# Kernel tuning notes

Hardware: AMD Instinct MI355X
Metric: run time of the kernel (lower is better)

## Reference

```python
import jax, jax.numpy as jnp
from jax import lax
import numpy as np

IN, H, OUT = 2, 8, 2

def _lstm_layer(x_tbi, w_ih, w_hh, b_ih, b_hh, return_seq):
    # x_tbi: [T, B, in]; w_ih: [4H, in]; w_hh: [4H, H]; biases: [4H]
    T, B, _ = x_tbi.shape
    Hd = w_hh.shape[1]
    # precompute input projection for all timesteps (batched GEMM)
    xs = jnp.einsum('tbi,gi->tbg', x_tbi, w_ih) + (b_ih + b_hh)  # [T, B, 4H]

    def step(carry, xt):
        h, c = carry
        gates = xt + h @ w_hh.T  # [B, 4H]
        i, f, g, o = jnp.split(gates, 4, axis=-1)  # PyTorch gate order i,f,g,o
        i = jax.nn.sigmoid(i)
        f = jax.nn.sigmoid(f)
        g = jnp.tanh(g)
        o = jax.nn.sigmoid(o)
        c = f * c + i * g
        h = o * jnp.tanh(c)
        return (h, c), (h if return_seq else None)

    init = (jnp.zeros((B, Hd), x_tbi.dtype), jnp.zeros((B, Hd), x_tbi.dtype))
    (h_last, _), hs = lax.scan(step, init, xs)
    return hs if return_seq else h_last


def setup_inputs() -> dict:
    key = jax.random.key(0)
    ks = jax.random.split(key, 12)
    s_in = 1.0 / np.sqrt(H)  # PyTorch LSTM init scale U(-1/sqrt(H), 1/sqrt(H))
    def u(k, shape):
        return jax.random.uniform(k, shape, jnp.float32, -s_in, s_in)
    inp = {
        'input': jax.random.normal(ks[0], (32768, 256, IN), jnp.float32),
        'w_ih0': u(ks[1], (4 * H, IN)),
        'w_hh0': u(ks[2], (4 * H, H)),
        'b_ih0': u(ks[3], (4 * H,)),
        'b_hh0': u(ks[4], (4 * H,)),
        'w_ih1': u(ks[5], (4 * H, H)),
        'w_hh1': u(ks[6], (4 * H, H)),
        'b_ih1': u(ks[7], (4 * H,)),
        'b_hh1': u(ks[8], (4 * H,)),
        'w_mlp': u(ks[9], (OUT, H)),
        'b_mlp': u(ks[10], (OUT,)),
    }
    return inp


def reference(input, w_ih0, w_hh0, b_ih0, b_hh0, w_ih1, w_hh1, b_ih1, b_hh1, w_mlp, b_mlp):
    x = jnp.transpose(input, (1, 0, 2))  # [T, B, 2] (batch_first -> time major)
    hs0 = _lstm_layer(x, w_ih0, w_hh0, b_ih0, b_hh0, return_seq=True)   # [T, B, H]
    h1 = _lstm_layer(hs0, w_ih1, w_hh1, b_ih1, b_hh1, return_seq=False)  # [B, H] final step
    return h1 @ w_mlp.T + b_mlp  # [B, 2]
```

## Files before the change

kernel.cpp:

```cpp
#include <hip/hip_runtime.h>


#define TT 256
#define NB 32768

typedef _Float16 half_t;
typedef _Float16 v2h  __attribute__((ext_vector_type(2)));
typedef _Float16 v8h  __attribute__((ext_vector_type(8)));
typedef __fp16   q2h  __attribute__((ext_vector_type(2)));
typedef float    v16f __attribute__((ext_vector_type(16)));
typedef int      v4i  __attribute__((ext_vector_type(4)));

__device__ __forceinline__ v2h pkrtz(float a, float b) {
    q2h r = __builtin_amdgcn_cvt_pkrtz(a, b);
    return __builtin_bit_cast(v2h, r);
}
__device__ __forceinline__ int pk_rtn(float a, float b) {
    v2h v; v.x = (half_t)a; v.y = (half_t)b;
    return __builtin_bit_cast(int, v);
}
__device__ __forceinline__ float rcp_(float x) { return __builtin_amdgcn_rcpf(x); }
__device__ __forceinline__ float ex2_(float x) { return __builtin_amdgcn_exp2f(x); }

__global__ __launch_bounds__(256) void lstm2_mfma32(
    const float* __restrict__ input,
    const float* __restrict__ w_ih0,
    const float* __restrict__ w_hh0,
    const float* __restrict__ b_ih0,
    const float* __restrict__ b_hh0,
    const float* __restrict__ w_ih1,
    const float* __restrict__ w_hh1,
    const float* __restrict__ b_ih1,
    const float* __restrict__ b_hh1,
    const float* __restrict__ w_mlp,
    const float* __restrict__ b_mlp,
    float* __restrict__ out)
{
    const int lane = threadIdx.x & 63;
    const int wave = blockIdx.x * 4 + (threadIdx.x >> 6);
    const int col  = lane & 31;
    const int hf   = lane >> 5;
    const int elem = wave * 32 + col;

    const float L2E = 1.44269504088896f;
    const float NS  = -L2E;
    const float NT2 = -2.0f * L2E;

    const int   row = col;
    const float sA  = (row >= 16 && row < 24) ? NT2 : NS;

    v8h A0, A1;
    if (hf == 0) {
#pragma unroll
        for (int j = 0; j < 8; ++j) {
            A0[j] = (half_t)(sA * w_hh0[row * 8 + j]);
            A1[j] = (half_t)(sA * w_ih1[row * 8 + j]);
        }
    } else {
        A0[0] = (half_t)(sA * w_ih0[row * 2 + 0]);
        A0[1] = (half_t)(sA * w_ih0[row * 2 + 1]);
        A0[2] = A0[0];
        A0[3] = A0[1];
#pragma unroll
        for (int j = 4; j < 8; ++j) A0[j] = (half_t)0.f;
#pragma unroll
        for (int j = 0; j < 8; ++j) A1[j] = (half_t)(sA * w_hh1[row * 8 + j]);
    }

    v16f bias0, bias1;
#pragma unroll
    for (int r = 0; r < 16; ++r) {
        const int   rw = (r & 3) + 8 * (r >> 2) + 4 * hf;
        const float s  = (rw >= 16 && rw < 24) ? NT2 : NS;
        bias0[r] = s * (b_ih0[rw] + b_hh0[rw]);
        bias1[r] = s * (b_ih1[rw] + b_hh1[rw]);
    }

    float c0[4] = {0.f, 0.f, 0.f, 0.f}, c1[4] = {0.f, 0.f, 0.f, 0.f};
    int h0w0 = 0, h0w1 = 0, h0w2 = 0, h0w3 = 0;
    int h1w0 = 0, h1w1 = 0, h1w2 = 0, h1w3 = 0;
    float h1f[4] = {0.f, 0.f, 0.f, 0.f};

    const float4* __restrict__ xp =
        reinterpret_cast<const float4*>(input + (size_t)elem * (TT * 2));

    auto cell = [&](float x0, float x1) {
        v2h xh = pkrtz(x0, x1);
        v2h xl = pkrtz(x0 - (float)xh.x, x1 - (float)xh.y);
        const int xw0 = __builtin_bit_cast(int, xh);
        const int xw1 = __builtin_bit_cast(int, xl);

        v4i b;
        b.x = hf ? xw0 : h0w0;
        b.y = hf ? xw1 : h0w1;
        b.z = hf ? 0   : h0w2;
        b.w = hf ? 0   : h0w3;
        v16f acc = __builtin_amdgcn_mfma_f32_32x32x16_f16(
            A0, __builtin_bit_cast(v8h, b), bias0, 0, 0, 0);

        float nh[4];
#pragma unroll
        for (int j = 0; j < 4; ++j) {
            float ig = rcp_(1.f + ex2_(acc[j]));
            float fg = rcp_(1.f + ex2_(acc[4 + j]));
            float gg = __builtin_fmaf(2.f, rcp_(1.f + ex2_(acc[8 + j])), -1.f);
            float og = rcp_(1.f + ex2_(acc[12 + j]));
            c0[j] = __builtin_fmaf(fg, c0[j], ig * gg);
            float t = __builtin_fmaf(2.f, rcp_(1.f + ex2_(c0[j] * NT2)), -1.f);
            nh[j] = og * t;
        }
        {
            int own0 = pk_rtn(nh[0], nh[1]);
            int own1 = pk_rtn(nh[2], nh[3]);
            int oth0 = __shfl_xor(own0, 32);
            int oth1 = __shfl_xor(own1, 32);
            h0w0 = hf ? oth0 : own0;
            h0w1 = hf ? oth1 : own1;
            h0w2 = hf ? own0 : oth0;
            h0w3 = hf ? own1 : oth1;
        }

        b.x = hf ? h1w0 : h0w0;
        b.y = hf ? h1w1 : h0w1;
        b.z = hf ? h1w2 : h0w2;
        b.w = hf ? h1w3 : h0w3;
        acc = __builtin_amdgcn_mfma_f32_32x32x16_f16(
            A1, __builtin_bit_cast(v8h, b), bias1, 0, 0, 0);

#pragma unroll
        for (int j = 0; j < 4; ++j) {
            float ig = rcp_(1.f + ex2_(acc[j]));
            float fg = rcp_(1.f + ex2_(acc[4 + j]));
            float gg = __builtin_fmaf(2.f, rcp_(1.f + ex2_(acc[8 + j])), -1.f);
            float og = rcp_(1.f + ex2_(acc[12 + j]));
            c1[j] = __builtin_fmaf(fg, c1[j], ig * gg);
            float t = __builtin_fmaf(2.f, rcp_(1.f + ex2_(c1[j] * NT2)), -1.f);
            h1f[j] = og * t;
        }
        {
            int own0 = pk_rtn(h1f[0], h1f[1]);
            int own1 = pk_rtn(h1f[2], h1f[3]);
            int oth0 = __shfl_xor(own0, 32);
            int oth1 = __shfl_xor(own1, 32);
            h1w0 = hf ? oth0 : own0;
            h1w1 = hf ? oth1 : own1;
            h1w2 = hf ? own0 : oth0;
            h1w3 = hf ? own1 : oth1;
        }
    };

    float4 cur = xp[0];
#pragma unroll 1
    for (int it = 0; it < TT / 2; ++it) {
        float4 nxt = xp[(it + 1) & (TT / 2 - 1)];
        cell(cur.x, cur.y);
        cell(cur.z, cur.w);
        cur = nxt;
    }

    const int q = 4 * hf;
    float p0 = 0.f, p1 = 0.f;
#pragma unroll
    for (int j = 0; j < 4; ++j) {
        p0 += w_mlp[q + j] * h1f[j];
        p1 += w_mlp[8 + q + j] * h1f[j];
    }
    p0 += __shfl_xor(p0, 32);
    p1 += __shfl_xor(p1, 32);
    if (hf == 0) {
        out[elem * 2 + 0] = p0 + b_mlp[0];
        out[elem * 2 + 1] = p1 + b_mlp[1];
    }
}

extern "C" void kernel_launch(void* const* d_in, const int* in_sizes, int n_in,
                              void* d_out, int out_size, void* d_ws, size_t ws_size,
                              hipStream_t stream) {
    const float* input = (const float*)d_in[0];
    const float* w_ih0 = (const float*)d_in[1];
    const float* w_hh0 = (const float*)d_in[2];
    const float* b_ih0 = (const float*)d_in[3];
    const float* b_hh0 = (const float*)d_in[4];
    const float* w_ih1 = (const float*)d_in[5];
    const float* w_hh1 = (const float*)d_in[6];
    const float* b_ih1 = (const float*)d_in[7];
    const float* b_hh1 = (const float*)d_in[8];
    const float* w_mlp = (const float*)d_in[9];
    const float* b_mlp = (const float*)d_in[10];
    float* out = (float*)d_out;

    dim3 block(256);
    dim3 grid(NB / 128);
    lstm2_mfma32<<<grid, block, 0, stream>>>(input, w_ih0, w_hh0, b_ih0, b_hh0,
                                             w_ih1, w_hh1, b_ih1, b_hh1,
                                             w_mlp, b_mlp, out);
}
```

Measured before the change: 262.4 us.

## Split LSTM layers across producer/consumer waves with chunked LDS pipeline

Each block now holds two wave pairs. In each pair, one wave runs layer 0 over a 16-step chunk and writes the h0 values to double-buffered shared memory, while the other wave runs layer 1 on the previous chunk. This breaks the serial layer0→layer1 dependency inside one wave, so the two layers' MFMA and transcendental chains can overlap on separate waves. In exchange it needs twice as many waves per element, block-wide barriers every chunk, LDS traffic, and one extra pipeline phase.

```diff
diff --git a/kernel.cpp b/kernel.cpp
--- a/kernel.cpp
+++ b/kernel.cpp
@@ -1,8 +1,10 @@
 #include <hip/hip_runtime.h>
 
 
-#define TT 256
-#define NB 32768
+#define TT  256
+#define NB  32768
+#define CH  16
+#define NCH (TT / CH)
 
 typedef _Float16 half_t;
 typedef _Float16 v2h  __attribute__((ext_vector_type(2)));
@@ -22,7 +24,7 @@
 __device__ __forceinline__ float rcp_(float x) { return __builtin_amdgcn_rcpf(x); }
 __device__ __forceinline__ float ex2_(float x) { return __builtin_amdgcn_exp2f(x); }
 
-__global__ __launch_bounds__(256) void lstm2_mfma32(
+__global__ __launch_bounds__(256) void lstm2_pipe(
     const float* __restrict__ input,
     const float* __restrict__ w_ih0,
     const float* __restrict__ w_hh0,
@@ -37,139 +39,145 @@
     float* __restrict__ out)
 {
     const int lane = threadIdx.x & 63;
-    const int wave = blockIdx.x * 4 + (threadIdx.x >> 6);
+    const int wv   = threadIdx.x >> 6;
+    const int grp  = wv & 1;
+    const int role = wv >> 1;
     const int col  = lane & 31;
     const int hf   = lane >> 5;
-    const int elem = wave * 32 + col;
+    const int elem = blockIdx.x * 64 + grp * 32 + col;
+
+    __shared__ int h0buf[2][2][CH][128];
 
     const float L2E = 1.44269504088896f;
     const float NS  = -L2E;
     const float NT2 = -2.0f * L2E;
-
-    const int   row = col;
-    const float sA  = (row >= 16 && row < 24) ? NT2 : NS;
-
-    v8h A0, A1;
-    if (hf == 0) {
-#pragma unroll
-        for (int j = 0; j < 8; ++j) {
-            A0[j] = (half_t)(sA * w_hh0[row * 8 + j]);
-            A1[j] = (half_t)(sA * w_ih1[row * 8 + j]);
+    const float sA  = (col >= 16 && col < 24) ? NT2 : NS;
+
+    v8h A;
+    if (role == 0) {
+        if (hf == 0) {
+#pragma unroll
+            for (int j = 0; j < 8; ++j) A[j] = (half_t)(sA * w_hh0[col * 8 + j]);
+        } else {
+            A[0] = (half_t)(sA * w_ih0[col * 2 + 0]);
+            A[1] = (half_t)(sA * w_ih0[col * 2 + 1]);
+            A[2] = A[0]; A[3] = A[1];
+#pragma unroll
+            for (int j = 4; j < 8; ++j) A[j] = (half_t)0.f;
         }
     } else {
-        A0[0] = (half_t)(sA * w_ih0[row * 2 + 0]);
-        A0[1] = (half_t)(sA * w_ih0[row * 2 + 1]);
-        A0[2] = A0[0];
-        A0[3] = A0[1];
-#pragma unroll
-        for (int j = 4; j < 8; ++j) A0[j] = (half_t)0.f;
-#pragma unroll
-        for (int j = 0; j < 8; ++j) A1[j] = (half_t)(sA * w_hh1[row * 8 + j]);
-    }
-
-    v16f bias0, bias1;
+        const float* wsrc = hf ? w_hh1 : w_ih1;
+#pragma unroll
+        for (int j = 0; j < 8; ++j) A[j] = (half_t)(sA * wsrc[col * 8 + j]);
+    }
+
+    v16f bias;
 #pragma unroll
     for (int r = 0; r < 16; ++r) {
         const int   rw = (r & 3) + 8 * (r >> 2) + 4 * hf;
         const float s  = (rw >= 16 && rw < 24) ? NT2 : NS;
-        bias0[r] = s * (b_ih0[rw] + b_hh0[rw]);
-        bias1[r] = s * (b_ih1[rw] + b_hh1[rw]);
-    }
-
-    float c0[4] = {0.f, 0.f, 0.f, 0.f}, c1[4] = {0.f, 0.f, 0.f, 0.f};
-    int h0w0 = 0, h0w1 = 0, h0w2 = 0, h0w3 = 0;
-    int h1w0 = 0, h1w1 = 0, h1w2 = 0, h1w3 = 0;
-    float h1f[4] = {0.f, 0.f, 0.f, 0.f};
+        bias[r] = (role == 0) ? s * (b_ih0[rw] + b_hh0[rw])
+                              : s * (b_ih1[rw] + b_hh1[rw]);
+    }
+
+    float c[4] = {0.f, 0.f, 0.f, 0.f};
+    int   hw0 = 0, hw1 = 0, hw2 = 0, hw3 = 0;
+    float hq[4] = {0.f, 0.f, 0.f, 0.f};
 
     const float4* __restrict__ xp =
         reinterpret_cast<const float4*>(input + (size_t)elem * (TT * 2));
 
-    auto cell = [&](float x0, float x1) {
-        v2h xh = pkrtz(x0, x1);
-        v2h xl = pkrtz(x0 - (float)xh.x, x1 - (float)xh.y);
-        const int xw0 = __builtin_bit_cast(int, xh);
-        const int xw1 = __builtin_bit_cast(int, xl);
-
-        v4i b;
-        b.x = hf ? xw0 : h0w0;
-        b.y = hf ? xw1 : h0w1;
-        b.z = hf ? 0   : h0w2;
-        b.w = hf ? 0   : h0w3;
-        v16f acc = __builtin_amdgcn_mfma_f32_32x32x16_f16(
-            A0, __builtin_bit_cast(v8h, b), bias0, 0, 0, 0);
-
-        float nh[4];
+    auto gates = [&](const v16f& acc, float* hout) {
 #pragma unroll
         for (int j = 0; j < 4; ++j) {
             float ig = rcp_(1.f + ex2_(acc[j]));
             float fg = rcp_(1.f + ex2_(acc[4 + j]));
             float gg = __builtin_fmaf(2.f, rcp_(1.f + ex2_(acc[8 + j])), -1.f);
             float og = rcp_(1.f + ex2_(acc[12 + j]));
-            c0[j] = __builtin_fmaf(fg, c0[j], ig * gg);
-            float t = __builtin_fmaf(2.f, rcp_(1.f + ex2_(c0[j] * NT2)), -1.f);
-            nh[j] = og * t;
-        }
-        {
-            int own0 = pk_rtn(nh[0], nh[1]);
-            int own1 = pk_rtn(nh[2], nh[3]);
-            int oth0 = __shfl_xor(own0, 32);
-            int oth1 = __shfl_xor(own1, 32);
-            h0w0 = hf ? oth0 : own0;
-            h0w1 = hf ? oth1 : own1;
-            h0w2 = hf ? own0 : oth0;
-            h0w3 = hf ? own1 : oth1;
-        }
-
-        b.x = hf ? h1w0 : h0w0;
-        b.y = hf ? h1w1 : h0w1;
-        b.z = hf ? h1w2 : h0w2;
-        b.w = hf ? h1w3 : h0w3;
-        acc = __builtin_amdgcn_mfma_f32_32x32x16_f16(
-            A1, __builtin_bit_cast(v8h, b), bias1, 0, 0, 0);
-
+            c[j] = __builtin_fmaf(fg, c[j], ig * gg);
+            float t = __builtin_fmaf(2.f, rcp_(1.f + ex2_(c[j] * NT2)), -1.f);
+            hout[j] = og * t;
+        }
+    };
+
+    for (int ph = 0; ph <= NCH; ++ph) {
+        if (role == 0) {
+            if (ph < NCH) {
+                int* lb = &h0buf[grp][ph & 1][0][0];
+#pragma unroll 2
+                for (int s2 = 0; s2 < CH / 2; ++s2) {
+                    float4 xv = xp[ph * (CH / 2) + s2];
+#pragma unroll
+                    for (int half = 0; half < 2; ++half) {
+                        float x0 = half ? xv.z : xv.x;
+                        float x1 = half ? xv.w : xv.y;
+                        v2h xh = pkrtz(x0, x1);
+                        v2h xl = pkrtz(x0 - (float)xh.x, x1 - (float)xh.y);
+                        int xw0 = __builtin_bit_cast(int, xh);
+                        int xw1 = __builtin_bit_cast(int, xl);
+                        v4i b;
+                        b.x = hf ? xw0 : hw0;
+                        b.y = hf ? xw1 : hw1;
+                        b.z = hf ? 0   : hw2;
+                        b.w = hf ? 0   : hw3;
+                        v16f acc = __builtin_amdgcn_mfma_f32_32x32x16_f16(
+                            A, __builtin_bit_cast(v8h, b), bias, 0, 0, 0);
+                        float nh[4];
+                        gates(acc, nh);
+                        int own0 = pk_rtn(nh[0], nh[1]);
+                        int own1 = pk_rtn(nh[2], nh[3]);
+                        int2 st; st.x = own0; st.y = own1;
+                        *reinterpret_cast<int2*>(
+                            &lb[(2 * s2 + half) * 128 + col * 4 + hf * 2]) = st;
+                        int oth0 = __shfl_xor(own0, 32);
+                        int oth1 = __shfl_xor(own1, 32);
+                        hw0 = hf ? oth0 : own0;
+                        hw1 = hf ? oth1 : own1;
+                        hw2 = hf ? own0 : oth0;
+                        hw3 = hf ? own1 : oth1;
+                    }
+                }
+            }
+        } else if (ph > 0) {
+            const int* lb = &h0buf[grp][(ph - 1) & 1][0][0];
+#pragma unroll 2
+            for (int s = 0; s < CH; ++s) {
+                v4i hh = *reinterpret_cast<const v4i*>(&lb[s * 128 + col * 4]);
+                v4i b;
+                b.x = hf ? hw0 : hh.x;
+                b.y = hf ? hw1 : hh.y;
+                b.z = hf ? hw2 : hh.z;
+                b.w = hf ? hw3 : hh.w;
+                v16f acc = __builtin_amdgcn_mfma_f32_32x32x16_f16(
+                    A, __builtin_bit_cast(v8h, b), bias, 0, 0, 0);
+                gates(acc, hq);
+                int own0 = pk_rtn(hq[0], hq[1]);
+                int own1 = pk_rtn(hq[2], hq[3]);
+                int oth0 = __shfl_xor(own0, 32);
+                int oth1 = __shfl_xor(own1, 32);
+                hw0 = hf ? oth0 : own0;
+                hw1 = hf ? oth1 : own1;
+                hw2 = hf ? own0 : oth0;
+                hw3 = hf ? own1 : oth1;
+            }
+        }
+        __syncthreads();
+    }
+
+    if (role == 1) {
+        const int q = 4 * hf;
+        float p0 = 0.f, p1 = 0.f;
 #pragma unroll
         for (int j = 0; j < 4; ++j) {
-            float ig = rcp_(1.f + ex2_(acc[j]));
-            float fg = rcp_(1.f + ex2_(acc[4 + j]));
-            float gg = __builtin_fmaf(2.f, rcp_(1.f + ex2_(acc[8 + j])), -1.f);
-            float og = rcp_(1.f + ex2_(acc[12 + j]));
-            c1[j] = __builtin_fmaf(fg, c1[j], ig * gg);
-            float t = __builtin_fmaf(2.f, rcp_(1.f + ex2_(c1[j] * NT2)), -1.f);
-            h1f[j] = og * t;
-        }
-        {
-            int own0 = pk_rtn(h1f[0], h1f[1]);
-            int own1 = pk_rtn(h1f[2], h1f[3]);
-            int oth0 = __shfl_xor(own0, 32);
-            int oth1 = __shfl_xor(own1, 32);
-            h1w0 = hf ? oth0 : own0;
-            h1w1 = hf ? oth1 : own1;
-            h1w2 = hf ? own0 : oth0;
-            h1w3 = hf ? own1 : oth1;
-        }
-    };
-
-    float4 cur = xp[0];
-#pragma unroll 1
-    for (int it = 0; it < TT / 2; ++it) {
-        float4 nxt = xp[(it + 1) & (TT / 2 - 1)];
-        cell(cur.x, cur.y);
-        cell(cur.z, cur.w);
-        cur = nxt;
-    }
-
-    const int q = 4 * hf;
-    float p0 = 0.f, p1 = 0.f;
-#pragma unroll
-    for (int j = 0; j < 4; ++j) {
-        p0 += w_mlp[q + j] * h1f[j];
-        p1 += w_mlp[8 + q + j] * h1f[j];
-    }
-    p0 += __shfl_xor(p0, 32);
-    p1 += __shfl_xor(p1, 32);
-    if (hf == 0) {
-        out[elem * 2 + 0] = p0 + b_mlp[0];
-        out[elem * 2 + 1] = p1 + b_mlp[1];
+            p0 += w_mlp[q + j] * hq[j];
+            p1 += w_mlp[8 + q + j] * hq[j];
+        }
+        p0 += __shfl_xor(p0, 32);
+        p1 += __shfl_xor(p1, 32);
+        if (hf == 0) {
+            out[elem * 2 + 0] = p0 + b_mlp[0];
+            out[elem * 2 + 1] = p1 + b_mlp[1];
+        }
     }
 }
 
@@ -190,8 +198,8 @@
     float* out = (float*)d_out;
 
     dim3 block(256);
-    dim3 grid(NB / 128);
-    lstm2_mfma32<<<grid, block, 0, stream>>>(input, w_ih0, w_hh0, b_ih0, b_hh0,
-                                             w_ih1, w_hh1, b_ih1, b_hh1,
-                                             w_mlp, b_mlp, out);
-}
+    dim3 grid(NB / 64);
+    lstm2_pipe<<<grid, block, 0, stream>>>(input, w_ih0, w_hh0, b_ih0, b_hh0,
+                                           w_ih1, w_hh1, b_ih1, b_hh1,
+                                           w_mlp, b_mlp, out);
+}
```

After: 256.6 us. 1.02x faster.

## Skew layer pipeline and remap MFMA K-split to drop lane shuffles

Applied to the files above, without the earlier changes.

The two LSTM layers are now software-pipelined with a one-step skew. Layer 0 at step t and layer 1 at step t-1 are issued as independent MFMAs, then both gate activations run, so the dependency chains can overlap. The A-operand layout is reorganized so each half-wave supplies K-slices that match the h values it already holds. This removes the per-step cross-half shuffles and selects that the old layout needed. A prologue and epilogue handle the skew, and the rearranged K layout must stay numerically equivalent.

```diff
diff --git a/kernel.cpp b/kernel.cpp
--- a/kernel.cpp
+++ b/kernel.cpp
@@ -22,7 +22,7 @@
 __device__ __forceinline__ float rcp_(float x) { return __builtin_amdgcn_rcpf(x); }
 __device__ __forceinline__ float ex2_(float x) { return __builtin_amdgcn_exp2f(x); }
 
-__global__ __launch_bounds__(256) void lstm2_mfma32(
+__global__ __launch_bounds__(256) void lstm2_dual(
     const float* __restrict__ input,
     const float* __restrict__ w_ih0,
     const float* __restrict__ w_hh0,
@@ -45,26 +45,22 @@
     const float L2E = 1.44269504088896f;
     const float NS  = -L2E;
     const float NT2 = -2.0f * L2E;
-
     const int   row = col;
     const float sA  = (row >= 16 && row < 24) ? NT2 : NS;
 
     v8h A0, A1;
+#pragma unroll
+    for (int j = 0; j < 4; ++j) {
+        A0[j]     = (half_t)(sA * w_hh0[row * 8 + 4 * hf + j]);
+        A1[j]     = (half_t)(sA * w_ih1[row * 8 + 4 * hf + j]);
+        A1[4 + j] = (half_t)(sA * w_hh1[row * 8 + 4 * hf + j]);
+    }
     if (hf == 0) {
-#pragma unroll
-        for (int j = 0; j < 8; ++j) {
-            A0[j] = (half_t)(sA * w_hh0[row * 8 + j]);
-            A1[j] = (half_t)(sA * w_ih1[row * 8 + j]);
-        }
+        A0[4] = (half_t)(sA * w_ih0[row * 2 + 0]);
+        A0[5] = (half_t)(sA * w_ih0[row * 2 + 1]);
+        A0[6] = A0[4]; A0[7] = A0[5];
     } else {
-        A0[0] = (half_t)(sA * w_ih0[row * 2 + 0]);
-        A0[1] = (half_t)(sA * w_ih0[row * 2 + 1]);
-        A0[2] = A0[0];
-        A0[3] = A0[1];
-#pragma unroll
-        for (int j = 4; j < 8; ++j) A0[j] = (half_t)0.f;
-#pragma unroll
-        for (int j = 0; j < 8; ++j) A1[j] = (half_t)(sA * w_hh1[row * 8 + j]);
+        A0[4] = A0[5] = A0[6] = A0[7] = (half_t)0.f;
     }
 
     v16f bias0, bias1;
@@ -77,85 +73,78 @@
     }
 
     float c0[4] = {0.f, 0.f, 0.f, 0.f}, c1[4] = {0.f, 0.f, 0.f, 0.f};
-    int h0w0 = 0, h0w1 = 0, h0w2 = 0, h0w3 = 0;
-    int h1w0 = 0, h1w1 = 0, h1w2 = 0, h1w3 = 0;
+    int   h0w0 = 0, h0w1 = 0;
+    int   h1w0 = 0, h1w1 = 0;
     float h1f[4] = {0.f, 0.f, 0.f, 0.f};
 
     const float4* __restrict__ xp =
         reinterpret_cast<const float4*>(input + (size_t)elem * (TT * 2));
 
-    auto cell = [&](float x0, float x1) {
-        v2h xh = pkrtz(x0, x1);
-        v2h xl = pkrtz(x0 - (float)xh.x, x1 - (float)xh.y);
-        const int xw0 = __builtin_bit_cast(int, xh);
-        const int xw1 = __builtin_bit_cast(int, xl);
-
-        v4i b;
-        b.x = hf ? xw0 : h0w0;
-        b.y = hf ? xw1 : h0w1;
-        b.z = hf ? 0   : h0w2;
-        b.w = hf ? 0   : h0w3;
-        v16f acc = __builtin_amdgcn_mfma_f32_32x32x16_f16(
-            A0, __builtin_bit_cast(v8h, b), bias0, 0, 0, 0);
-
-        float nh[4];
+    auto gates = [&](const v16f& acc, float* c, float* hout) {
 #pragma unroll
         for (int j = 0; j < 4; ++j) {
             float ig = rcp_(1.f + ex2_(acc[j]));
             float fg = rcp_(1.f + ex2_(acc[4 + j]));
             float gg = __builtin_fmaf(2.f, rcp_(1.f + ex2_(acc[8 + j])), -1.f);
             float og = rcp_(1.f + ex2_(acc[12 + j]));
-            c0[j] = __builtin_fmaf(fg, c0[j], ig * gg);
-            float t = __builtin_fmaf(2.f, rcp_(1.f + ex2_(c0[j] * NT2)), -1.f);
-            nh[j] = og * t;
-        }
-        {
-            int own0 = pk_rtn(nh[0], nh[1]);
-            int own1 = pk_rtn(nh[2], nh[3]);
-            int oth0 = __shfl_xor(own0, 32);
-            int oth1 = __shfl_xor(own1, 32);
-            h0w0 = hf ? oth0 : own0;
-            h0w1 = hf ? oth1 : own1;
-            h0w2 = hf ? own0 : oth0;
-            h0w3 = hf ? own1 : oth1;
-        }
-
-        b.x = hf ? h1w0 : h0w0;
-        b.y = hf ? h1w1 : h0w1;
-        b.z = hf ? h1w2 : h0w2;
-        b.w = hf ? h1w3 : h0w3;
-        acc = __builtin_amdgcn_mfma_f32_32x32x16_f16(
-            A1, __builtin_bit_cast(v8h, b), bias1, 0, 0, 0);
-
-#pragma unroll
-        for (int j = 0; j < 4; ++j) {
-            float ig = rcp_(1.f + ex2_(acc[j]));
-            float fg = rcp_(1.f + ex2_(acc[4 + j]));
-            float gg = __builtin_fmaf(2.f, rcp_(1.f + ex2_(acc[8 + j])), -1.f);
-            float og = rcp_(1.f + ex2_(acc[12 + j]));
-            c1[j] = __builtin_fmaf(fg, c1[j], ig * gg);
-            float t = __builtin_fmaf(2.f, rcp_(1.f + ex2_(c1[j] * NT2)), -1.f);
-            h1f[j] = og * t;
-        }
-        {
-            int own0 = pk_rtn(h1f[0], h1f[1]);
-            int own1 = pk_rtn(h1f[2], h1f[3]);
-            int oth0 = __shfl_xor(own0, 32);
-            int oth1 = __shfl_xor(own1, 32);
-            h1w0 = hf ? oth0 : own0;
-            h1w1 = hf ? oth1 : own1;
-            h1w2 = hf ? own0 : oth0;
-            h1w3 = hf ? own1 : oth1;
+            c[j] = __builtin_fmaf(fg, c[j], ig * gg);
+            float t = __builtin_fmaf(2.f, rcp_(1.f + ex2_(c[j] * NT2)), -1.f);
+            hout[j] = og * t;
         }
     };
 
-    float4 cur = xp[0];
+    auto packx = [&](float x0, float x1) -> int2 {
+        v2h xh = pkrtz(x0, x1);
+        v2h xl = pkrtz(x0 - (float)xh.x, x1 - (float)xh.y);
+        int2 r; r.x = __builtin_bit_cast(int, xh); r.y = __builtin_bit_cast(int, xl);
+        return r;
+    };
+
+    auto mfmaL0 = [&](int2 xw) -> v16f {
+        v4i b; b.x = h0w0; b.y = h0w1; b.z = xw.x; b.w = xw.y;
+        return __builtin_amdgcn_mfma_f32_32x32x16_f16(
+            A0, __builtin_bit_cast(v8h, b), bias0, 0, 0, 0);
+    };
+    auto mfmaL1 = [&]() -> v16f {
+        v4i b; b.x = h0w0; b.y = h0w1; b.z = h1w0; b.w = h1w1;
+        return __builtin_amdgcn_mfma_f32_32x32x16_f16(
+            A1, __builtin_bit_cast(v8h, b), bias1, 0, 0, 0);
+    };
+    auto actL0 = [&](const v16f& acc) {
+        float nh[4];
+        gates(acc, c0, nh);
+        h0w0 = pk_rtn(nh[0], nh[1]);
+        h0w1 = pk_rtn(nh[2], nh[3]);
+    };
+    auto actL1 = [&](const v16f& acc) {
+        gates(acc, c1, h1f);
+        h1w0 = pk_rtn(h1f[0], h1f[1]);
+        h1w1 = pk_rtn(h1f[2], h1f[3]);
+    };
+
+    auto dual = [&](float x0, float x1) {
+        int2 xw = packx(x0, x1);
+        v16f a0 = mfmaL0(xw);
+        v16f a1 = mfmaL1();
+        actL0(a0);
+        actL1(a1);
+    };
+
+    {
+        float4 xv = xp[0];
+        v16f a0 = mfmaL0(packx(xv.x, xv.y));
+        actL0(a0);
+        dual(xv.z, xv.w);
+    }
 #pragma unroll 1
-    for (int it = 0; it < TT / 2; ++it) {
-        float4 nxt = xp[(it + 1) & (TT / 2 - 1)];
-        cell(cur.x, cur.y);
-        cell(cur.z, cur.w);
-        cur = nxt;
+    for (int it = 1; it < TT / 2; ++it) {
+        float4 xv = xp[it];
+        dual(xv.x, xv.y);
+        dual(xv.z, xv.w);
+    }
+    {
+        v16f a1 = mfmaL1();
+        actL1(a1);
     }
 
     const int q = 4 * hf;
@@ -191,7 +180,7 @@
 
     dim3 block(256);
     dim3 grid(NB / 128);
-    lstm2_mfma32<<<grid, block, 0, stream>>>(input, w_ih0, w_hh0, b_ih0, b_hh0,
-                                             w_ih1, w_hh1, b_ih1, b_hh1,
-                                             w_mlp, b_mlp, out);
+    lstm2_dual<<<grid, block, 0, stream>>>(input, w_ih0, w_hh0, b_ih0, b_hh0,
+                                           w_ih1, w_hh1, b_ih1, b_hh1,
+                                           w_mlp, b_mlp, out);
 }
```

Measured after the change: 240.8 us. -8.2%, faster.
